# Optimization experiments

Hardware: AMD Instinct MI355X
Metric: run time of the kernel (lower is better)

Reference implementation:

```python
import jax, jax.numpy as jnp
import numpy as np

B, H, CO, NV, NQ = 16, 1024, 512, 2048, 2048

def setup_inputs() -> dict:
    key = jax.random.key(0)
    ks = jax.random.split(key, 7)
    return {
        "V": jax.random.normal(ks[0], (B, H, NV), dtype=jnp.float32),
        "Q": jax.random.normal(ks[1], (B, NQ, H), dtype=jnp.float32),
        "W_b": jax.random.normal(ks[2], (H, H), dtype=jnp.float32),
        "W_v": jax.random.normal(ks[3], (CO, H), dtype=jnp.float32),
        "W_q": jax.random.normal(ks[4], (CO, H), dtype=jnp.float32),
        "w_hv": jax.random.normal(ks[5], (CO, 1), dtype=jnp.float32),
        "w_hq": jax.random.normal(ks[6], (CO, 1), dtype=jnp.float32),
    }

def reference(V, Q, W_b, W_v, W_q, w_hv, w_hq):
    # C = Q @ (W_b @ V): [B, Nq, Nv]
    WbV = jnp.einsum('hk,bkv->bhv', W_b, V)
    C = jnp.einsum('bqh,bhv->bqv', Q, WbV)
    WvV = jnp.einsum('ch,bhv->bcv', W_v, V)          # [B, CO, Nv]
    WqQt = jnp.einsum('ch,bqh->bcq', W_q, Q)         # [B, CO, Nq]
    H_v = jnp.tanh(WvV + jnp.einsum('bcq,bqv->bcv', WqQt, C))   # [B, CO, Nv]
    H_q = jnp.tanh(WqQt + jnp.einsum('bcv,bqv->bcq', WvV, C))   # [B, CO, Nq]
    a_v = jax.nn.softmax(jnp.einsum('c,bcv->bv', w_hv[:, 0], H_v), axis=-1)[:, None, :]  # [B,1,Nv]
    a_q = jax.nn.softmax(jnp.einsum('c,bcq->bq', w_hq[:, 0], H_q), axis=-1)[:, None, :]  # [B,1,Nq]
    v = jnp.einsum('bv,bhv->bh', a_v[:, 0], V)   # [B, H]
    q = jnp.einsum('bq,bqh->bh', a_q[:, 0], Q)   # [B, H]
    return (a_v, a_q, v, q)
```

## Files before the change

kernel.cpp:

```cpp
#include <hip/hip_runtime.h>
#include <math.h>

#define Bn  16
#define Hd  1024
#define COn 512
#define NVn 2048
#define NQn 2048

#define BM 128
#define BN 128
#define BK 16
#define LDT 132

typedef unsigned short u16;
typedef __attribute__((ext_vector_type(8))) short short8;
typedef __attribute__((ext_vector_type(4))) float floatx4;

__device__ __forceinline__ float fast_tanh(float x) {
    float ax = fabsf(x);
    float e  = __expf(2.0f * ax);
    float t  = 1.0f - 2.0f / (e + 1.0f);
    return copysignf(t, x);
}

__device__ __forceinline__ u16 f32_to_bf16(float x) {
    unsigned u = __float_as_uint(x);
    unsigned r = (u + 0x7fffu + ((u >> 16) & 1u)) >> 16;
    return (u16)r;
}
__device__ __forceinline__ float bf16_to_f32(u16 h) {
    return __uint_as_float(((unsigned)h) << 16);
}

template <bool LOGITS>
__global__ __launch_bounds__(256) void mm3(
    const u16* __restrict__ Ahp, const u16* __restrict__ Alp, long batchA, int ldA,
    const u16* __restrict__ Bhp, const u16* __restrict__ Blp, long batchB, int ldB,
    int N, int K,
    const float* __restrict__ bias,
    u16* __restrict__ Ch, u16* __restrict__ Cl, long batchC,
    const float* __restrict__ w, float* __restrict__ logits)
{
    __shared__ u16 Ah[128 * 32], Al[128 * 32], Bh[128 * 32], Bl[128 * 32];
    const int tid = threadIdx.x;
    const int b   = blockIdx.z;
    const int m0  = blockIdx.y * 128;
    const int n0  = blockIdx.x * 128;
    const u16* Ahb = Ahp + (long)b * batchA;
    const u16* Alb = Alp + (long)b * batchA;
    const u16* Bhb = Bhp + (long)b * batchB;
    const u16* Blb = Blp + (long)b * batchB;
    const int wave = tid >> 6, lane = tid & 63, quad = lane >> 4, l16 = lane & 15;
    const int wm = (wave >> 1) * 64, wn = (wave & 1) * 64;
    floatx4 acc[4][4] = {};

    for (int k0 = 0; k0 < K; k0 += 32) {
#pragma unroll
        for (int i = 0; i < 2; ++i) {
            int c = i * 256 + tid;
            int row = c >> 2, ko = (c & 3) * 8;
            long ga = (long)(m0 + row) * ldA + k0 + ko;
            long gb = (long)(n0 + row) * ldB + k0 + ko;
            *(short8*)&Ah[row * 32 + ko] = *(const short8*)&Ahb[ga];
            *(short8*)&Al[row * 32 + ko] = *(const short8*)&Alb[ga];
            *(short8*)&Bh[row * 32 + ko] = *(const short8*)&Bhb[gb];
            *(short8*)&Bl[row * 32 + ko] = *(const short8*)&Blb[gb];
        }
        __syncthreads();
        short8 ah[4], al[4], bh[4], bl[4];
#pragma unroll
        for (int t4 = 0; t4 < 4; ++t4) {
            int am = wm + t4 * 16 + l16;
            ah[t4] = *(const short8*)&Ah[am * 32 + quad * 8];
            al[t4] = *(const short8*)&Al[am * 32 + quad * 8];
            int bn = wn + t4 * 16 + l16;
            bh[t4] = *(const short8*)&Bh[bn * 32 + quad * 8];
            bl[t4] = *(const short8*)&Bl[bn * 32 + quad * 8];
        }
#pragma unroll
        for (int mt = 0; mt < 4; ++mt)
#pragma unroll
            for (int nt = 0; nt < 4; ++nt) {
                floatx4 a0 = acc[mt][nt];
                a0 = __builtin_amdgcn_mfma_f32_16x16x32_bf16(ah[mt], bh[nt], a0, 0, 0, 0);
                a0 = __builtin_amdgcn_mfma_f32_16x16x32_bf16(ah[mt], bl[nt], a0, 0, 0, 0);
                a0 = __builtin_amdgcn_mfma_f32_16x16x32_bf16(al[mt], bh[nt], a0, 0, 0, 0);
                acc[mt][nt] = a0;
            }
        __syncthreads();
    }

    if constexpr (!LOGITS) {
        u16* Chb = Ch + (long)b * batchC;
        u16* Clb = Cl + (long)b * batchC;
#pragma unroll
        for (int mt = 0; mt < 4; ++mt)
#pragma unroll
            for (int nt = 0; nt < 4; ++nt)
#pragma unroll
                for (int r = 0; r < 4; ++r) {
                    int row = m0 + wm + mt * 16 + quad * 4 + r;
                    int col = n0 + wn + nt * 16 + l16;
                    float x = acc[mt][nt][r];
                    if (bias) x += bias[(long)row * N + col];
                    u16 h = f32_to_bf16(x);
                    u16 l = f32_to_bf16(x - bf16_to_f32(h));
                    Chb[(long)row * N + col] = h;
                    Clb[(long)row * N + col] = l;
                }
    } else {
        float cs[4] = {};
#pragma unroll
        for (int nt = 0; nt < 4; ++nt)
#pragma unroll
            for (int mt = 0; mt < 4; ++mt)
#pragma unroll
                for (int r = 0; r < 4; ++r) {
                    int row = m0 + wm + mt * 16 + quad * 4 + r;
                    cs[nt] = fmaf(w[row], fast_tanh(acc[mt][nt][r]), cs[nt]);
                }
        float* red = (float*)Ah;
        const int r8 = (wave >> 1) * 4 + quad;
#pragma unroll
        for (int nt = 0; nt < 4; ++nt)
            red[r8 * 128 + wn + nt * 16 + l16] = cs[nt];
        __syncthreads();
        if (tid < 128) {
            float s = 0.f;
#pragma unroll
            for (int r = 0; r < 8; ++r) s += red[r * 128 + tid];
            atomicAdd(logits + (long)b * N + n0 + tid, s);
        }
    }
}

__global__ __launch_bounds__(256) void split_kernel(
    const float* __restrict__ X, u16* __restrict__ Xh, u16* __restrict__ Xl)
{
    long i0 = ((long)blockIdx.x * 256 + threadIdx.x) * 4;
    float4 v = *(const float4*)(X + i0);
    float xs[4] = {v.x, v.y, v.z, v.w};
    u16 h[4], l[4];
#pragma unroll
    for (int i = 0; i < 4; ++i) {
        h[i] = f32_to_bf16(xs[i]);
        l[i] = f32_to_bf16(xs[i] - bf16_to_f32(h[i]));
    }
    *(ushort4*)(Xh + i0) = *(ushort4*)h;
    *(ushort4*)(Xl + i0) = *(ushort4*)l;
}

__global__ __launch_bounds__(256) void tsplit_kernel(
    const float* __restrict__ src, u16* __restrict__ dh, u16* __restrict__ dl,
    int R, int C)
{
    __shared__ float tile[64][65];
    const int b = blockIdx.z;
    const int r0 = blockIdx.x * 64, c0 = blockIdx.y * 64;
    const float* S = src + (long)b * R * C;
    const int t = threadIdx.x;
    const int lr = t >> 2, lc0 = (t & 3) * 16;
#pragma unroll
    for (int i = 0; i < 4; ++i)
        *(float4*)&tile[lr][lc0 + i * 4] =
            *(const float4*)(S + (long)(r0 + lr) * C + c0 + lc0 + i * 4);
    __syncthreads();
    u16 hbuf[16], lbuf[16];
#pragma unroll
    for (int i = 0; i < 16; ++i) {
        float x = tile[lc0 + i][lr];
        u16 hi = f32_to_bf16(x);
        hbuf[i] = hi;
        lbuf[i] = f32_to_bf16(x - bf16_to_f32(hi));
    }
    long o = (long)b * R * C + (long)(c0 + lr) * R + r0 + lc0;
    *(short8*)(dh + o)     = *(short8*)&hbuf[0];
    *(short8*)(dh + o + 8) = *(short8*)&hbuf[8];
    *(short8*)(dl + o)     = *(short8*)&lbuf[0];
    *(short8*)(dl + o + 8) = *(short8*)&lbuf[8];
}

template <bool LOGITS>
__global__ __launch_bounds__(256) void gemm_core(
    const float* __restrict__ A, const float* __restrict__ Bm, float* __restrict__ C,
    const float* __restrict__ bias,
    int M, int N, int K,
    int sAm, int sAk, long batchA,
    int sBk, int sBn, long batchB,
    long batchC,
    const float* __restrict__ w, float* __restrict__ logits)
{
    __shared__ float As[BK][LDT];
    __shared__ float Bs[BK][LDT];
    const int tid = threadIdx.x;
    const int b   = blockIdx.z;
    const int m0  = blockIdx.y * BM;
    const int n0  = blockIdx.x * BN;
    const float* Ab = A  + (long)b * batchA;
    const float* Bb = Bm + (long)b * batchB;
    const int tm = tid >> 4, tn = tid & 15;
    float acc[8][8] = {};

    for (int k0 = 0; k0 < K; k0 += BK) {
        if (sAk == 1) {
#pragma unroll
            for (int i = 0; i < 2; ++i) {
                int idx = tid + i * 256;
                int m = idx >> 2, kg = (idx & 3) * 4;
                float4 v = *(const float4*)(Ab + (long)(m0 + m) * sAm + k0 + kg);
                As[kg+0][m] = v.x; As[kg+1][m] = v.y; As[kg+2][m] = v.z; As[kg+3][m] = v.w;
            }
        } else {
#pragma unroll
            for (int i = 0; i < 2; ++i) {
                int idx = tid + i * 256;
                int k = idx >> 5, mg = (idx & 31) * 4;
                float4 v = *(const float4*)(Ab + (long)(k0 + k) * sAk + m0 + mg);
                *(float4*)&As[k][mg] = v;
            }
        }
        if (sBn == 1) {
#pragma unroll
            for (int i = 0; i < 2; ++i) {
                int idx = tid + i * 256;
                int k = idx >> 5, ng = (idx & 31) * 4;
                float4 v = *(const float4*)(Bb + (long)(k0 + k) * sBk + n0 + ng);
                *(float4*)&Bs[k][ng] = v;
            }
        } else {
#pragma unroll
            for (int i = 0; i < 2; ++i) {
                int idx = tid + i * 256;
                int n = idx >> 2, kg = (idx & 3) * 4;
                float4 v = *(const float4*)(Bb + (long)(n0 + n) * sBn + k0 + kg);
                Bs[kg+0][n] = v.x; Bs[kg+1][n] = v.y; Bs[kg+2][n] = v.z; Bs[kg+3][n] = v.w;
            }
        }
        __syncthreads();
#pragma unroll
        for (int kk = 0; kk < BK; ++kk) {
            float a[8], bv[8];
            *(float4*)&a[0]  = *(const float4*)&As[kk][tm * 4];
            *(float4*)&a[4]  = *(const float4*)&As[kk][64 + tm * 4];
            *(float4*)&bv[0] = *(const float4*)&Bs[kk][tn * 4];
            *(float4*)&bv[4] = *(const float4*)&Bs[kk][64 + tn * 4];
#pragma unroll
            for (int i = 0; i < 8; ++i)
#pragma unroll
                for (int j = 0; j < 8; ++j)
                    acc[i][j] = fmaf(a[i], bv[j], acc[i][j]);
        }
        __syncthreads();
    }

    if constexpr (!LOGITS) {
        float* Cb = C + (long)b * batchC;
#pragma unroll
        for (int i = 0; i < 8; ++i) {
            int row = m0 + (i >> 2) * 64 + tm * 4 + (i & 3);
            float* crow = Cb + (long)row * N + n0;
            float4 o0 = {acc[i][0], acc[i][1], acc[i][2], acc[i][3]};
            float4 o1 = {acc[i][4], acc[i][5], acc[i][6], acc[i][7]};
            if (bias) {
                const float* brow = bias + (long)row * N + n0;
                float4 b0 = *(const float4*)(brow + tn * 4);
                float4 b1 = *(const float4*)(brow + 64 + tn * 4);
                o0.x += b0.x; o0.y += b0.y; o0.z += b0.z; o0.w += b0.w;
                o1.x += b1.x; o1.y += b1.y; o1.z += b1.z; o1.w += b1.w;
            }
            *(float4*)(crow + tn * 4) = o0;
            *(float4*)(crow + 64 + tn * 4) = o1;
        }
    } else {
        float wv[8];
#pragma unroll
        for (int i = 0; i < 8; ++i) wv[i] = w[m0 + (i >> 2) * 64 + tm * 4 + (i & 3)];
        float cs[8];
#pragma unroll
        for (int j = 0; j < 8; ++j) {
            float s = 0.f;
#pragma unroll
            for (int i = 0; i < 8; ++i) s = fmaf(wv[i], fast_tanh(acc[i][j]), s);
            cs[j] = s;
        }
        __syncthreads();
        *(float4*)&As[tm][tn * 4]      = *(float4*)&cs[0];
        *(float4*)&As[tm][64 + tn * 4] = *(float4*)&cs[4];
        __syncthreads();
        if (tid < 128) {
            float s = 0.f;
#pragma unroll
            for (int r = 0; r < 16; ++r) s += As[r][tid];
            atomicAdd(logits + (long)b * N + n0 + tid, s);
        }
    }
}

__global__ __launch_bounds__(256) void softmax_kernel(
    const float* __restrict__ lv, const float* __restrict__ lq, float* __restrict__ out)
{
    const int b = blockIdx.x;
    const int which = blockIdx.y;
    const float* x = (which == 0 ? lv : lq) + (long)b * 2048;
    float* o = out + (long)which * (Bn * 2048) + (long)b * 2048;
    const int tid = threadIdx.x;
    __shared__ float sm[4], ss[4];

    float m = -3.4e38f;
    for (int i = tid; i < 2048; i += 256) m = fmaxf(m, x[i]);
    for (int off = 32; off > 0; off >>= 1) m = fmaxf(m, __shfl_down(m, off));
    if ((tid & 63) == 0) sm[tid >> 6] = m;
    __syncthreads();
    m = fmaxf(fmaxf(sm[0], sm[1]), fmaxf(sm[2], sm[3]));

    float s = 0.f;
    for (int i = tid; i < 2048; i += 256) s += expf(x[i] - m);
    for (int off = 32; off > 0; off >>= 1) s += __shfl_down(s, off);
    if ((tid & 63) == 0) ss[tid >> 6] = s;
    __syncthreads();
    s = ss[0] + ss[1] + ss[2] + ss[3];
    float inv = 1.0f / s;
    for (int i = tid; i < 2048; i += 256) o[i] = expf(x[i] - m) * inv;
}

__global__ __launch_bounds__(256) void vout_kernel(
    const float* __restrict__ V, const float* __restrict__ av, float* __restrict__ vout)
{
    const int wave = threadIdx.x >> 6, lane = threadIdx.x & 63;
    const long idx = (long)blockIdx.x * 4 + wave;
    const int b = (int)(idx >> 10);
    const int h = (int)(idx & 1023);
    const float* vp = V + ((long)b * Hd + h) * NVn;
    const float* ap = av + (long)b * NVn;
    float s = 0.f;
    for (int i = lane; i < NVn; i += 64) s = fmaf(ap[i], vp[i], s);
    for (int off = 32; off > 0; off >>= 1) s += __shfl_down(s, off);
    if (lane == 0) vout[idx] = s;
}

__global__ __launch_bounds__(256) void qout_kernel(
    const float* __restrict__ Q, const float* __restrict__ aq, float* __restrict__ qout)
{
    const int h  = blockIdx.x * 256 + threadIdx.x;
    const int b  = blockIdx.z;
    const int q0 = blockIdx.y * 256;
    const float* qp = Q + (long)b * NQn * Hd;
    const float* ap = aq + (long)b * NQn + q0;
    float s = 0.f;
    for (int q = 0; q < 256; ++q) s = fmaf(ap[q], qp[(long)(q0 + q) * Hd + h], s);
    atomicAdd(qout + (long)b * Hd + h, s);
}

extern "C" void kernel_launch(void* const* d_in, const int* in_sizes, int n_in,
                              void* d_out, int out_size, void* d_ws, size_t ws_size,
                              hipStream_t stream) {
    const float* V    = (const float*)d_in[0];
    const float* Q    = (const float*)d_in[1];
    const float* W_b  = (const float*)d_in[2];
    const float* W_v  = (const float*)d_in[3];
    const float* W_q  = (const float*)d_in[4];
    const float* w_hv = (const float*)d_in[5];
    const float* w_hq = (const float*)d_in[6];
    float* out = (float*)d_out;
    dim3 blk(256);

    const long BIG  = (long)Bn * Hd * NVn;
    const long GEL  = (long)Bn * Hd * Hd;
    const long TEL  = (long)Bn * COn * Hd;
    const long WQE  = (long)COn * Hd;
    const long WBE  = (long)Hd * Hd;

    u16* ws16 = (u16*)d_ws;
    u16* R1h  = ws16;            u16* R1l  = R1h + BIG;
    u16* Gh   = R1l + BIG;       u16* Gl   = Gh + GEL;
    u16* Th   = Gl + GEL;        u16* Tl   = Th + TEL;
    u16* Uh   = Gh;              u16* Ul   = Gh + TEL;
    u16* Wqh  = Tl + TEL;        u16* Wql  = Wqh + WQE;
    u16* Wvh  = Wql + WQE;       u16* Wvl  = Wvh + WQE;
    u16* Wbh  = Wvl + WQE;       u16* Wbl  = Wbh + WBE;
    u16* WbTh = Wbl + WBE;       u16* WbTl = WbTh + WBE;
    float* lv = (float*)(WbTl + WBE);
    float* lq = lv + Bn * NVn;
    const size_t need = (size_t)((u16*)(lq + Bn * NQn) - ws16) * 2;

    float* vout_p = out + 2 * Bn * NVn;
    float* qout_p = vout_p + Bn * Hd;

    if (ws_size >= need) {
        hipMemsetAsync(lv, 0, (size_t)(Bn * NVn + Bn * NQn) * sizeof(float), stream);
        hipMemsetAsync(qout_p, 0, (size_t)Bn * Hd * sizeof(float), stream);

        split_kernel<<<dim3((unsigned)(WQE / 1024)), blk, 0, stream>>>(W_q, Wqh, Wql);
        split_kernel<<<dim3((unsigned)(WQE / 1024)), blk, 0, stream>>>(W_v, Wvh, Wvl);
        split_kernel<<<dim3((unsigned)(WBE / 1024)), blk, 0, stream>>>(W_b, Wbh, Wbl);
        tsplit_kernel<<<dim3(Hd / 64, Hd / 64, 1), blk, 0, stream>>>(W_b, WbTh, WbTl, Hd, Hd);

        tsplit_kernel<<<dim3(NQn / 64, Hd / 64, Bn), blk, 0, stream>>>(Q, R1h, R1l, NQn, Hd);
        mm3<false><<<dim3(Hd / 128, Hd / 128, Bn), blk, 0, stream>>>(
            R1h, R1l, (long)Hd * NQn, NQn,  R1h, R1l, (long)Hd * NQn, NQn,
            Hd, NQn, nullptr, Gh, Gl, (long)Hd * Hd, nullptr, nullptr);
        mm3<false><<<dim3(Hd / 128, COn / 128, Bn), blk, 0, stream>>>(
            Wqh, Wql, 0L, Hd,  Gh, Gl, (long)Hd * Hd, Hd,
            Hd, Hd, nullptr, Th, Tl, (long)COn * Hd, nullptr, nullptr);
        mm3<false><<<dim3(Hd / 128, COn / 128, Bn), blk, 0, stream>>>(
            Th, Tl, (long)COn * Hd, Hd,  WbTh, WbTl, 0L, Hd,
            Hd, Hd, W_v, Uh, Ul, (long)COn * Hd, nullptr, nullptr);
        tsplit_kernel<<<dim3(Hd / 64, NVn / 64, Bn), blk, 0, stream>>>(V, R1h, R1l, Hd, NVn);
        mm3<true><<<dim3(NVn / 128, COn / 128, Bn), blk, 0, stream>>>(
            Uh, Ul, (long)COn * Hd, Hd,  R1h, R1l, (long)NVn * Hd, Hd,
            NVn, Hd, nullptr, nullptr, nullptr, 0L, w_hv, lv);

        split_kernel<<<dim3((unsigned)(BIG / 1024)), blk, 0, stream>>>(V, R1h, R1l);
        mm3<false><<<dim3(Hd / 128, Hd / 128, Bn), blk, 0, stream>>>(
            R1h, R1l, (long)Hd * NVn, NVn,  R1h, R1l, (long)Hd * NVn, NVn,
            Hd, NVn, nullptr, Gh, Gl, (long)Hd * Hd, nullptr, nullptr);
        mm3<false><<<dim3(Hd / 128, COn / 128, Bn), blk, 0, stream>>>(
            Wvh, Wvl, 0L, Hd,  Gh, Gl, (long)Hd * Hd, Hd,
            Hd, Hd, nullptr, Th, Tl, (long)COn * Hd, nullptr, nullptr);
        mm3<false><<<dim3(Hd / 128, COn / 128, Bn), blk, 0, stream>>>(
            Th, Tl, (long)COn * Hd, Hd,  Wbh, Wbl, 0L, Hd,
            Hd, Hd, W_q, Uh, Ul, (long)COn * Hd, nullptr, nullptr);
        split_kernel<<<dim3((unsigned)(BIG / 1024)), blk, 0, stream>>>(Q, R1h, R1l);
        mm3<true><<<dim3(NQn / 128, COn / 128, Bn), blk, 0, stream>>>(
            Uh, Ul, (long)COn * Hd, Hd,  R1h, R1l, (long)NQn * Hd, Hd,
            NQn, Hd, nullptr, nullptr, nullptr, 0L, w_hq, lq);

        softmax_kernel<<<dim3(Bn, 2), blk, 0, stream>>>(lv, lq, out);
        vout_kernel<<<dim3(Bn * Hd / 4), blk, 0, stream>>>(V, out, vout_p);
        qout_kernel<<<dim3(Hd / 256, NQn / 256, Bn), blk, 0, stream>>>(Q, out + Bn * NVn, qout_p);
        return;
    }

    float* ws = (float*)d_ws;
    float* g  = ws;
    float* t  = g + GEL;
    float* u  = t + TEL;
    float* flv = u + TEL;
    float* flq = flv + Bn * NVn;

    hipMemsetAsync(flv, 0, (size_t)(Bn * NVn + Bn * NQn) * sizeof(float), stream);
    hipMemsetAsync(qout_p, 0, (size_t)Bn * Hd * sizeof(float), stream);

    gemm_core<false><<<dim3(Hd/BN, Hd/BM, Bn), blk, 0, stream>>>(Q, Q, g, nullptr,
        Hd, Hd, NQn, 1, Hd, (long)NQn*Hd, Hd, 1, (long)NQn*Hd, (long)Hd*Hd, nullptr, nullptr);
    gemm_core<false><<<dim3(Hd/BN, COn/BM, Bn), blk, 0, stream>>>(W_q, g, t, nullptr,
        COn, Hd, Hd, Hd, 1, 0L, Hd, 1, (long)Hd*Hd, (long)COn*Hd, nullptr, nullptr);
    gemm_core<false><<<dim3(Hd/BN, COn/BM, Bn), blk, 0, stream>>>(t, W_b, u, W_v,
        COn, Hd, Hd, Hd, 1, (long)COn*Hd, Hd, 1, 0L, (long)COn*Hd, nullptr, nullptr);
    gemm_core<true><<<dim3(NVn/BN, COn/BM, Bn), blk, 0, stream>>>(
        u, V, nullptr, nullptr, COn, NVn, Hd,
        Hd, 1, (long)COn*Hd, NVn, 1, (long)Hd*NVn, 0L, w_hv, flv);
    gemm_core<false><<<dim3(Hd/BN, Hd/BM, Bn), blk, 0, stream>>>(V, V, g, nullptr,
        Hd, Hd, NVn, NVn, 1, (long)Hd*NVn, 1, NVn, (long)Hd*NVn, (long)Hd*Hd, nullptr, nullptr);
    gemm_core<false><<<dim3(Hd/BN, COn/BM, Bn), blk, 0, stream>>>(W_v, g, t, nullptr,
        COn, Hd, Hd, Hd, 1, 0L, Hd, 1, (long)Hd*Hd, (long)COn*Hd, nullptr, nullptr);
    gemm_core<false><<<dim3(Hd/BN, COn/BM, Bn), blk, 0, stream>>>(t, W_b, u, W_q,
        COn, Hd, Hd, Hd, 1, (long)COn*Hd, 1, Hd, 0L, (long)COn*Hd, nullptr, nullptr);
    gemm_core<true><<<dim3(NQn/BN, COn/BM, Bn), blk, 0, stream>>>(
        u, Q, nullptr, nullptr, COn, NQn, Hd,
        Hd, 1, (long)COn*Hd, 1, Hd, (long)NQn*Hd, 0L, w_hq, flq);

    softmax_kernel<<<dim3(Bn, 2), blk, 0, stream>>>(flv, flq, out);
    vout_kernel<<<dim3(Bn * Hd / 4), blk, 0, stream>>>(V, out, vout_p);
    qout_kernel<<<dim3(Hd / 256, NQn / 256, Bn), blk, 0, stream>>>(Q, out + Bn * NVn, qout_p);
}
```

Measured before the change: 1.467 ms.

## Add 256x256-tile 8-wave MFMA GEMM with direct global-to-LDS double buffering

Result: faster. 1.275 ms (-13.1%).

```diff
diff --git a/kernel.cpp b/kernel.cpp
--- a/kernel.cpp
+++ b/kernel.cpp
@@ -30,6 +30,161 @@
 }
 __device__ __forceinline__ float bf16_to_f32(u16 h) {
     return __uint_as_float(((unsigned)h) << 16);
+}
+
+__device__ __forceinline__ void gload16(const u16* g, u16* l) {
+    __builtin_amdgcn_global_load_lds(
+        (__attribute__((address_space(1))) void*)(g),
+        (__attribute__((address_space(3))) void*)(l), 16, 0, 0);
+}
+
+template <bool LOGITS>
+__global__ __launch_bounds__(512, 2) void mm8p(
+    const u16* __restrict__ Ahp, const u16* __restrict__ Alp, long batchA, int ldA,
+    const u16* __restrict__ Bhp, const u16* __restrict__ Blp, long batchB, int ldB,
+    int N, int K, int gx, int gy,
+    const float* __restrict__ bias,
+    u16* __restrict__ Ch, u16* __restrict__ Cl, long batchC,
+    const float* __restrict__ w, float* __restrict__ logits)
+{
+    __shared__ u16 lds[2][4][256 * 32];
+
+    const int tid = threadIdx.x;
+    const int nwg = (int)gridDim.x;
+    int bid = (int)blockIdx.x;
+    {
+        int q = nwg >> 3, r = nwg & 7, xcd = bid & 7, idx = bid >> 3;
+        bid = (xcd < r ? xcd * (q + 1) : r * (q + 1) + (xcd - r) * q) + idx;
+    }
+    const int bpz = gx * gy;
+    const int b    = bid / bpz;
+    const int brem = bid - b * bpz;
+    const int m0 = (brem / gx) * 256;
+    const int n0 = (brem % gx) * 256;
+
+    const u16* Ahb = Ahp + (long)b * batchA;
+    const u16* Alb = Alp + (long)b * batchA;
+    const u16* Bhb = Bhp + (long)b * batchB;
+    const u16* Blb = Blp + (long)b * batchB;
+
+    const int wave = tid >> 6, lane = tid & 63;
+    const int quad = lane >> 4, l16 = lane & 15;
+    const int wm = (wave >> 2) * 128;
+    const int wn = (wave & 3) * 64;
+    const int aoff = quad * 8;
+
+    const int smat  = wave >> 1;
+    const int srow0 = (wave & 1) * 128;
+    const int srl   = lane >> 2;
+    const int ssl   = (lane & 3) * 8;
+    const u16* srcp = smat == 0 ? Ahb : smat == 1 ? Alb : smat == 2 ? Bhb : Blb;
+    const long sld  = (smat < 2) ? ldA : ldB;
+    const int rowbase = (smat < 2) ? m0 : n0;
+    const u16* sp = srcp + (long)(rowbase + srow0 + srl) * sld + ssl;
+
+    floatx4 acc[8][4] = {};
+
+#pragma unroll
+    for (int j = 0; j < 8; ++j)
+        gload16(sp + (long)j * 16 * sld, &lds[0][smat][(srow0 + j * 16) * 32]);
+    asm volatile("s_waitcnt vmcnt(0)" ::: "memory");
+    __builtin_amdgcn_s_barrier();
+
+    const int NT = K >> 5;
+    for (int t = 0; t < NT; ++t) {
+        const int  cur = t & 1;
+        const bool pf  = (t + 1 < NT);
+        const long k0n = (long)(t + 1) * 32;
+        const u16* Ah_ = &lds[cur][0][0];
+        const u16* Al_ = &lds[cur][1][0];
+        const u16* Bh_ = &lds[cur][2][0];
+        const u16* Bl_ = &lds[cur][3][0];
+        short8 bh[4], bl[4];
+#pragma unroll
+        for (int p = 0; p < 4; ++p) {
+            if (p == 0) {
+#pragma unroll
+                for (int nt = 0; nt < 4; ++nt) {
+                    const int br = (wn + nt * 16 + l16) * 32 + aoff;
+                    bh[nt] = *(const short8*)&Bh_[br];
+                    bl[nt] = *(const short8*)&Bl_[br];
+                }
+            }
+            const int ar0 = (wm + (2 * p) * 16 + l16) * 32 + aoff;
+            const int ar1 = ar0 + 16 * 32;
+            const short8 a0h = *(const short8*)&Ah_[ar0];
+            const short8 a0l = *(const short8*)&Al_[ar0];
+            const short8 a1h = *(const short8*)&Ah_[ar1];
+            const short8 a1l = *(const short8*)&Al_[ar1];
+            if (pf && p < 2) {
+                const int tb = cur ^ 1;
+#pragma unroll
+                for (int j = p * 4; j < p * 4 + 4; ++j)
+                    gload16(sp + (long)j * 16 * sld + k0n,
+                            &lds[tb][smat][(srow0 + j * 16) * 32]);
+            }
+            __builtin_amdgcn_s_barrier();
+            __builtin_amdgcn_s_setprio(1);
+#pragma unroll
+            for (int nt = 0; nt < 4; ++nt) {
+                floatx4 c0 = acc[2 * p][nt];
+                c0 = __builtin_amdgcn_mfma_f32_16x16x32_bf16(a0h, bh[nt], c0, 0, 0, 0);
+                c0 = __builtin_amdgcn_mfma_f32_16x16x32_bf16(a0h, bl[nt], c0, 0, 0, 0);
+                c0 = __builtin_amdgcn_mfma_f32_16x16x32_bf16(a0l, bh[nt], c0, 0, 0, 0);
+                acc[2 * p][nt] = c0;
+                floatx4 c1 = acc[2 * p + 1][nt];
+                c1 = __builtin_amdgcn_mfma_f32_16x16x32_bf16(a1h, bh[nt], c1, 0, 0, 0);
+                c1 = __builtin_amdgcn_mfma_f32_16x16x32_bf16(a1h, bl[nt], c1, 0, 0, 0);
+                c1 = __builtin_amdgcn_mfma_f32_16x16x32_bf16(a1l, bh[nt], c1, 0, 0, 0);
+                acc[2 * p + 1][nt] = c1;
+            }
+            __builtin_amdgcn_s_setprio(0);
+            if (p == 3 && pf) asm volatile("s_waitcnt vmcnt(0)" ::: "memory");
+            __builtin_amdgcn_s_barrier();
+        }
+    }
+
+    if constexpr (!LOGITS) {
+        u16* Chb = Ch + (long)b * batchC;
+        u16* Clb = Cl + (long)b * batchC;
+#pragma unroll
+        for (int mt = 0; mt < 8; ++mt)
+#pragma unroll
+            for (int nt = 0; nt < 4; ++nt)
+#pragma unroll
+                for (int r = 0; r < 4; ++r) {
+                    const int row = m0 + wm + mt * 16 + quad * 4 + r;
+                    const int col = n0 + wn + nt * 16 + l16;
+                    float x = acc[mt][nt][r];
+                    if (bias) x += bias[(long)row * N + col];
+                    const u16 h = f32_to_bf16(x);
+                    Chb[(long)row * N + col] = h;
+                    Clb[(long)row * N + col] = f32_to_bf16(x - bf16_to_f32(h));
+                }
+    } else {
+        float cs[4] = {};
+#pragma unroll
+        for (int nt = 0; nt < 4; ++nt)
+#pragma unroll
+            for (int mt = 0; mt < 8; ++mt)
+#pragma unroll
+                for (int r = 0; r < 4; ++r) {
+                    const int row = m0 + wm + mt * 16 + quad * 4 + r;
+                    cs[nt] = fmaf(w[row], fast_tanh(acc[mt][nt][r]), cs[nt]);
+                }
+        float* red = (float*)&lds[0][0][0];
+        const int r8 = (wave >> 2) * 4 + quad;
+#pragma unroll
+        for (int nt = 0; nt < 4; ++nt)
+            red[r8 * 256 + wn + nt * 16 + l16] = cs[nt];
+        __syncthreads();
+        if (tid < 256) {
+            float s = 0.f;
+#pragma unroll
+            for (int r = 0; r < 8; ++r) s += red[r * 256 + tid];
+            atomicAdd(logits + (long)b * N + n0 + tid, s);
+        }
+    }
 }
 
 template <bool LOGITS>
@@ -396,9 +551,10 @@
         tsplit_kernel<<<dim3(Hd / 64, Hd / 64, 1), blk, 0, stream>>>(W_b, WbTh, WbTl, Hd, Hd);
 
         tsplit_kernel<<<dim3(NQn / 64, Hd / 64, Bn), blk, 0, stream>>>(Q, R1h, R1l, NQn, Hd);
-        mm3<false><<<dim3(Hd / 128, Hd / 128, Bn), blk, 0, stream>>>(
+        mm8p<false><<<dim3((Hd / 256) * (Hd / 256) * Bn), dim3(512), 0, stream>>>(
             R1h, R1l, (long)Hd * NQn, NQn,  R1h, R1l, (long)Hd * NQn, NQn,
-            Hd, NQn, nullptr, Gh, Gl, (long)Hd * Hd, nullptr, nullptr);
+            Hd, NQn, Hd / 256, Hd / 256,
+            nullptr, Gh, Gl, (long)Hd * Hd, nullptr, nullptr);
         mm3<false><<<dim3(Hd / 128, COn / 128, Bn), blk, 0, stream>>>(
             Wqh, Wql, 0L, Hd,  Gh, Gl, (long)Hd * Hd, Hd,
             Hd, Hd, nullptr, Th, Tl, (long)COn * Hd, nullptr, nullptr);
@@ -406,14 +562,16 @@
             Th, Tl, (long)COn * Hd, Hd,  WbTh, WbTl, 0L, Hd,
             Hd, Hd, W_v, Uh, Ul, (long)COn * Hd, nullptr, nullptr);
         tsplit_kernel<<<dim3(Hd / 64, NVn / 64, Bn), blk, 0, stream>>>(V, R1h, R1l, Hd, NVn);
-        mm3<true><<<dim3(NVn / 128, COn / 128, Bn), blk, 0, stream>>>(
+        mm8p<true><<<dim3((NVn / 256) * (COn / 256) * Bn), dim3(512), 0, stream>>>(
             Uh, Ul, (long)COn * Hd, Hd,  R1h, R1l, (long)NVn * Hd, Hd,
-            NVn, Hd, nullptr, nullptr, nullptr, 0L, w_hv, lv);
+            NVn, Hd, NVn / 256, COn / 256,
+            nullptr, nullptr, nullptr, 0L, w_hv, lv);
 
         split_kernel<<<dim3((unsigned)(BIG / 1024)), blk, 0, stream>>>(V, R1h, R1l);
-        mm3<false><<<dim3(Hd / 128, Hd / 128, Bn), blk, 0, stream>>>(
+        mm8p<false><<<dim3((Hd / 256) * (Hd / 256) * Bn), dim3(512), 0, stream>>>(
             R1h, R1l, (long)Hd * NVn, NVn,  R1h, R1l, (long)Hd * NVn, NVn,
-            Hd, NVn, nullptr, Gh, Gl, (long)Hd * Hd, nullptr, nullptr);
+            Hd, NVn, Hd / 256, Hd / 256,
+            nullptr, Gh, Gl, (long)Hd * Hd, nullptr, nullptr);
         mm3<false><<<dim3(Hd / 128, COn / 128, Bn), blk, 0, stream>>>(
             Wvh, Wvl, 0L, Hd,  Gh, Gl, (long)Hd * Hd, Hd,
             Hd, Hd, nullptr, Th, Tl, (long)COn * Hd, nullptr, nullptr);
@@ -421,9 +579,10 @@
             Th, Tl, (long)COn * Hd, Hd,  Wbh, Wbl, 0L, Hd,
             Hd, Hd, W_q, Uh, Ul, (long)COn * Hd, nullptr, nullptr);
         split_kernel<<<dim3((unsigned)(BIG / 1024)), blk, 0, stream>>>(Q, R1h, R1l);
-        mm3<true><<<dim3(NQn / 128, COn / 128, Bn), blk, 0, stream>>>(
+        mm8p<true><<<dim3((NQn / 256) * (COn / 256) * Bn), dim3(512), 0, stream>>>(
             Uh, Ul, (long)COn * Hd, Hd,  R1h, R1l, (long)NQn * Hd, Hd,
-            NQn, Hd, nullptr, nullptr, nullptr, 0L, w_hq, lq);
+            NQn, Hd, NQn / 256, COn / 256,
+            nullptr, nullptr, nullptr, 0L, w_hq, lq);
 
         softmax_kernel<<<dim3(Bn, 2), blk, 0, stream>>>(lv, lq, out);
         vout_kernel<<<dim3(Bn * Hd / 4), blk, 0, stream>>>(V, out, vout_p);
```
